# Performance work log

Hardware: AMD Instinct MI355X
Metric: run time of the kernel (lower is better)

The kernel has to match this reference:

```python
import jax, jax.numpy as jnp
import numpy as np

B, S, E, H = 4, 1024, 1024, 16
HD = E // H
EPS = 1e-10


def setup_inputs() -> dict:
    key = jax.random.key(0)
    ks = jax.random.split(key, 10)
    w = lambda k: jax.random.normal(k, (E, E), jnp.float32) * 0.02
    b = lambda k: jax.random.normal(k, (E,), jnp.float32) * 0.02
    return {
        "query": jax.random.normal(ks[0], (B, S, E), jnp.float32),
        "Wq": w(ks[1]), "bq": b(ks[2]),
        "Wk": w(ks[3]), "bk": b(ks[4]),
        "Wv": w(ks[5]), "bv": b(ks[6]),
        "Wo": w(ks[7]), "bo": b(ks[8]),
        "alpha": jnp.array(1.0, jnp.float32),
    }


def reference(query, Wq, bq, Wk, bk, Wv, bv, Wo, bo, alpha):
    scale = 1.0 / np.sqrt(HD)
    # projections -> [B, H, S, HD]
    def heads(x, W, bias):
        return (x @ W.T + bias).reshape(B, S, H, HD).transpose(0, 2, 1, 3)
    Q = heads(query, Wq, bq)
    K = heads(query, Wk, bk)
    V = heads(query, Wv, bv)
    # raw scores [B, H, S, S]
    scores = jnp.einsum('bhqd,bhkd->bhqk', Q, K) * scale
    # 2D FFT over the (q, k) plane
    scores_fft = jnp.fft.fft2(scores, axes=(-2, -1))
    # spectral filter: exp(i * alpha * arctan(log|F| + eps))
    phase = alpha * jnp.arctan(jnp.log(jnp.abs(scores_fft) + EPS))
    filt = jnp.exp(1j * phase)
    scores_filtered = jnp.fft.ifft2(scores_fft * filt, axes=(-2, -1)).real
    # softmax over keys (dropout is identity at eval)
    attn = jax.nn.softmax(scores_filtered, axis=-1)
    ctx = jnp.einsum('bhqk,bhkd->bhqd', attn, V)
    ctx = ctx.transpose(0, 2, 1, 3).reshape(B, S, E)
    return ctx @ Wo.T + bo
```

## Files before the change

### kernel.cpp

```cpp
#include <hip/hip_runtime.h>
#include <hip/hip_fp16.h>


typedef __attribute__((ext_vector_type(8))) short short8;
typedef __attribute__((ext_vector_type(8))) _Float16 half8;
typedef __attribute__((ext_vector_type(4))) float f32x4;

#define PITCH 40
#define PITCH1 72

__device__ __forceinline__ float bf2f(short v) {
  return __uint_as_float(((unsigned)(unsigned short)v) << 16);
}
__device__ __forceinline__ short f2bf(float f) {
  unsigned u = __float_as_uint(f);
  u += 0x7FFFu + ((u >> 16) & 1u);
  return (short)(u >> 16);
}

__device__ __forceinline__ short8 ld8(const void* p, size_t idx, int isf32) {
  short8 r;
  if (isf32) {
    const float* f = (const float*)p + idx;
    float4 a = *(const float4*)f;
    float4 b = *(const float4*)(f + 4);
    r[0] = f2bf(a.x); r[1] = f2bf(a.y); r[2] = f2bf(a.z); r[3] = f2bf(a.w);
    r[4] = f2bf(b.x); r[5] = f2bf(b.y); r[6] = f2bf(b.z); r[7] = f2bf(b.w);
  } else {
    r = *(const short8*)((const short*)p + idx);
  }
  return r;
}
__device__ __forceinline__ float ldf(const void* p, int idx, int isf32) {
  return isf32 ? ((const float*)p)[idx] : bf2f(((const short*)p)[idx]);
}

__device__ __forceinline__ float2 cmul(float2 a, float2 b) {
  return make_float2(a.x * b.x - a.y * b.y, a.x * b.y + a.y * b.x);
}
__device__ __forceinline__ float2 cmulc(float2 a, float2 b) {
  return make_float2(a.x * b.x + a.y * b.y, a.y * b.x - a.x * b.y);
}
__device__ __forceinline__ float2 cadd(float2 a, float2 b) {
  return make_float2(a.x + b.x, a.y + b.y);
}
__device__ __forceinline__ float2 csub(float2 a, float2 b) {
  return make_float2(a.x - b.x, a.y - b.y);
}


template <int SGN>
__device__ __forceinline__ void dft16_dif(float2* x) {
  const float C16[8] = {1.f, 0.92387953f, 0.70710678f, 0.38268343f,
                        0.f, -0.38268343f, -0.70710678f, -0.92387953f};
  const float S16[8] = {0.f, 0.38268343f, 0.70710678f, 0.92387953f,
                        1.f, 0.92387953f, 0.70710678f, 0.38268343f};
#pragma unroll
  for (int h = 8; h >= 1; h >>= 1)
#pragma unroll
    for (int b = 0; b < 16; b += 2 * h)
#pragma unroll
      for (int i = 0; i < h; ++i) {
        const int e = i * (8 / h);
        float2 u = x[b + i], v = x[b + i + h];
        x[b + i] = cadd(u, v);
        float2 d = csub(u, v);
        float2 w = make_float2(C16[e], SGN > 0 ? S16[e] : -S16[e]);
        x[b + i + h] = (e == 0) ? d : cmul(d, w);
      }
}

__device__ __forceinline__ void dit16_inv(float2* x) {
  const float C16[8] = {1.f, 0.92387953f, 0.70710678f, 0.38268343f,
                        0.f, -0.38268343f, -0.70710678f, -0.92387953f};
  const float S16[8] = {0.f, 0.38268343f, 0.70710678f, 0.92387953f,
                        1.f, 0.92387953f, 0.70710678f, 0.38268343f};
#pragma unroll
  for (int h = 1; h <= 8; h <<= 1)
#pragma unroll
    for (int b = 0; b < 16; b += 2 * h)
#pragma unroll
      for (int i = 0; i < h; ++i) {
        const int e = i * (8 / h);
        float2 w = make_float2(C16[e], -S16[e]);
        float2 u = x[b + i];
        float2 vh = (e == 0) ? x[b + i + h] : cmulc(x[b + i + h], w);
        x[b + i] = cadd(u, vh);
        x[b + i + h] = csub(u, vh);
      }
}

template <int SGN>
__device__ __forceinline__ void midtw(float2* x, int lane) {
  const int rho[16] = {0, 8, 4, 12, 2, 10, 6, 14, 1, 9, 5, 13, 3, 11, 7, 15};
  float s, c;
  __sincosf((float)lane * 0.00613592315f, &s, &c);
  float2 w = make_float2(c, SGN > 0 ? s : -s);
  float2 run = w;
  x[8] = cmul(x[8], run);
#pragma unroll
  for (int e = 2; e < 16; ++e) {
    run = cmul(run, w);
    x[rho[e]] = cmul(x[rho[e]], run);
  }
}

template <int SGN>
__device__ __forceinline__ void xlane_dif(float2* x, int lane) {
#pragma unroll
  for (int h = 32; h >= 1; h >>= 1) {
    const int e = (lane & (h - 1)) * (32 / h);
    float s, c;
    __sincosf((float)e * 0.09817477042f, &s, &c);
    float2 w = make_float2(c, SGN > 0 ? s : -s);
    const bool hi = (lane & h) != 0;
#pragma unroll
    for (int r = 0; r < 16; ++r) {
      float2 t = x[r];
      float2 p;
      p.x = __shfl_xor(t.x, h, 64);
      p.y = __shfl_xor(t.y, h, 64);
      x[r] = hi ? cmul(csub(p, t), w) : cadd(t, p);
    }
  }
}

template <int SGN>
__device__ __forceinline__ void wfft1024_dif(float2* x, int lane) {
  dft16_dif<SGN>(x);
  midtw<SGN>(x, lane);
  xlane_dif<SGN>(x, lane);
}

template <int SGN>
__device__ __forceinline__ void midtw2(float2* x, float2* y, int lane) {
  const int rho[16] = {0, 8, 4, 12, 2, 10, 6, 14, 1, 9, 5, 13, 3, 11, 7, 15};
  float s, c;
  __sincosf((float)lane * 0.00613592315f, &s, &c);
  float2 w = make_float2(c, SGN > 0 ? s : -s);
  float2 run = w;
  x[8] = cmul(x[8], run);
  y[8] = cmul(y[8], run);
#pragma unroll
  for (int e = 2; e < 16; ++e) {
    run = cmul(run, w);
    x[rho[e]] = cmul(x[rho[e]], run);
    y[rho[e]] = cmul(y[rho[e]], run);
  }
}

__device__ __forceinline__ void midtw_inv2(float2* x, float2* y, int lane) {
  const int rho[16] = {0, 8, 4, 12, 2, 10, 6, 14, 1, 9, 5, 13, 3, 11, 7, 15};
  float s, c;
  __sincosf((float)lane * 0.00613592315f, &s, &c);
  float2 w = make_float2(c, -s);
  float2 run = w;
  x[8] = cmulc(x[8], run);
  y[8] = cmulc(y[8], run);
#pragma unroll
  for (int e = 2; e < 16; ++e) {
    run = cmul(run, w);
    x[rho[e]] = cmulc(x[rho[e]], run);
    y[rho[e]] = cmulc(y[rho[e]], run);
  }
}

template <int SGN>
__device__ __forceinline__ void xlane_dif2(float2* x, float2* y, int lane) {
#pragma unroll
  for (int h = 32; h >= 1; h >>= 1) {
    const int e = (lane & (h - 1)) * (32 / h);
    float s, c;
    __sincosf((float)e * 0.09817477042f, &s, &c);
    float2 w = make_float2(c, SGN > 0 ? s : -s);
    const bool hi = (lane & h) != 0;
#pragma unroll
    for (int r = 0; r < 16; ++r) {
      float2 t = x[r];
      float2 p;
      p.x = __shfl_xor(t.x, h, 64);
      p.y = __shfl_xor(t.y, h, 64);
      x[r] = hi ? cmul(csub(p, t), w) : cadd(t, p);
    }
#pragma unroll
    for (int r = 0; r < 16; ++r) {
      float2 t = y[r];
      float2 p;
      p.x = __shfl_xor(t.x, h, 64);
      p.y = __shfl_xor(t.y, h, 64);
      y[r] = hi ? cmul(csub(p, t), w) : cadd(t, p);
    }
  }
}

__device__ __forceinline__ void xlane_dit_inv2(float2* x, float2* y, int lane) {
#pragma unroll
  for (int h = 1; h <= 32; h <<= 1) {
    const int e = (lane & (h - 1)) * (32 / h);
    float s, c;
    __sincosf((float)e * 0.09817477042f, &s, &c);
    float2 w = make_float2(c, -s);
    const bool hi = (lane & h) != 0;
#pragma unroll
    for (int r = 0; r < 16; ++r) {
      float2 t = x[r];
      if (hi) t = cmulc(t, w);
      float2 p;
      p.x = __shfl_xor(t.x, h, 64);
      p.y = __shfl_xor(t.y, h, 64);
      x[r] = hi ? csub(p, t) : cadd(t, p);
    }
#pragma unroll
    for (int r = 0; r < 16; ++r) {
      float2 t = y[r];
      if (hi) t = cmulc(t, w);
      float2 p;
      p.x = __shfl_xor(t.x, h, 64);
      p.y = __shfl_xor(t.y, h, 64);
      y[r] = hi ? csub(p, t) : cadd(t, p);
    }
  }
}

template <int SGN>
__device__ __forceinline__ void wfft1024_dif2(float2* x, float2* y, int lane) {
  dft16_dif<SGN>(x);
  dft16_dif<SGN>(y);
  midtw2<SGN>(x, y, lane);
  xlane_dif2<SGN>(x, y, lane);
}
__device__ __forceinline__ void wfft1024_inv2(float2* x, float2* y, int lane) {
  xlane_dit_inv2(x, y, lane);
  midtw_inv2(x, y, lane);
  dit16_inv(x);
  dit16_inv(y);
}

__device__ __forceinline__ float gainw(float re, float im, float alpha, bool a1) {
  float mag2 = re * re + im * im;
  float t = 0.5f * __logf(mag2 + 1e-20f);
  if (a1) return __builtin_amdgcn_rsqf(fmaf(t, t, 1.0f)) * (1.0f / 1048576.0f);
  return __cosf(alpha * atanf(t)) * (1.0f / 1048576.0f);
}

__global__ void k0_detect(const unsigned* __restrict__ q,
                          const void* __restrict__ alphap, int* __restrict__ flags) {
  __shared__ float smax[256];
  __shared__ int szero[256];
  int t = threadIdx.x;
  float mx = 0.f; int zc = 0;
  for (int i = t; i < 16384; i += 256) {
    unsigned w = q[i];
    unsigned lo = w & 0xFFFFu;
    float v = fabsf(__uint_as_float(lo << 16));
    if (!(v <= 1e30f)) v = 1e30f;
    mx = fmaxf(mx, v);
    zc += (lo == 0u);
  }
  smax[t] = mx; szero[t] = zc;
  __syncthreads();
  for (int s = 128; s > 0; s >>= 1) {
    if (t < s) { smax[t] = fmaxf(smax[t], smax[t + s]); szero[t] += szero[t + s]; }
    __syncthreads();
  }
  if (t == 0) {
    int isf32 = (smax[0] > 100.f) || (szero[0] > 12288);
    flags[0] = isf32;
    float alpha = isf32 ? *(const float*)alphap : bf2f(*(const short*)alphap);
    ((float*)flags)[1] = alpha;
  }
}

__global__ __launch_bounds__(256) void k1_qkv(
    const void* __restrict__ x,
    const void* __restrict__ Wq, const void* __restrict__ bq,
    const void* __restrict__ Wk, const void* __restrict__ bk,
    const void* __restrict__ Wv, const void* __restrict__ bv,
    short* __restrict__ Qt, short* __restrict__ Kt, short* __restrict__ Vt,
    const int* __restrict__ flags)
{
  __shared__ __align__(16) char smem[128 * PITCH1 * 2 * 2];
  short* As = (short*)smem;
  short* Bs = As + 128 * PITCH1;
  short* Ct = (short*)smem;
  const int isf32 = flags[0];
  const int t = threadIdx.x;
  const int lb = blockIdx.x;
  const int m0 = ((lb & 7) * 4 + ((lb >> 3) & 3)) * 128;
  const int n0 = (lb >> 5) * 128;
  const int which = blockIdx.y;
  const void* __restrict__ W = (which == 0) ? Wq : (which == 1) ? Wk : Wv;
  const void* __restrict__ bias = (which == 0) ? bq : (which == 1) ? bk : bv;
  const int lane = t & 63, wvi = t >> 6;
  const int wr = wvi >> 1, wc = wvi & 1;
  const int lm = lane & 15, lq = lane >> 4;
  f32x4 acc[4][4] = {};

  for (int k0 = 0; k0 < 1024; k0 += 64) {
    __syncthreads();
#pragma unroll
    for (int i = 0; i < 4; ++i) {
      int l = t + i * 256;
      int row = l >> 3, kk = (l & 7) << 3;
      *(short8*)&As[row * PITCH1 + kk] = ld8(x, (size_t)(m0 + row) * 1024 + k0 + kk, isf32);
      *(short8*)&Bs[row * PITCH1 + kk] = ld8(W, (size_t)(n0 + row) * 1024 + k0 + kk, isf32);
    }
    __syncthreads();
#pragma unroll
    for (int kh = 0; kh < 2; ++kh) {
      short8 af[4], bf[4];
#pragma unroll
      for (int a = 0; a < 4; ++a)
        af[a] = *(const short8*)&As[(wr * 64 + a * 16 + lm) * PITCH1 + kh * 32 + lq * 8];
#pragma unroll
      for (int b = 0; b < 4; ++b)
        bf[b] = *(const short8*)&Bs[(wc * 64 + b * 16 + lm) * PITCH1 + kh * 32 + lq * 8];
#pragma unroll
      for (int a = 0; a < 4; ++a)
#pragma unroll
        for (int b = 0; b < 4; ++b)
          acc[a][b] = __builtin_amdgcn_mfma_f32_16x16x32_bf16(af[a], bf[b], acc[a][b], 0, 0, 0);
    }
  }

  __syncthreads();
#pragma unroll
  for (int a = 0; a < 4; ++a)
#pragma unroll
    for (int b = 0; b < 4; ++b) {
      int col = wc * 64 + b * 16 + lm;
      float bv_ = ldf(bias, n0 + col, isf32);
#pragma unroll
      for (int r = 0; r < 4; ++r) {
        int row = wr * 64 + a * 16 + lq * 4 + r;
        Ct[row * 136 + col] = f2bf(acc[a][b][r] + bv_);
      }
    }
  __syncthreads();

  short* __restrict__ O = (which == 0) ? Qt : (which == 1) ? Kt : Vt;
#pragma unroll
  for (int j = 0; j < 8; ++j) {
    int id = t + j * 256;
    int d128 = id & 127, sg = (id >> 7) * 8;
    short vals[8];
#pragma unroll
    for (int i = 0; i < 8; ++i) vals[i] = Ct[(sg + i) * 136 + d128];
    int col = n0 + d128;
    int h = col >> 6, d = col & 63;
    int bb = m0 >> 10, sbase = (m0 & 1023) + sg;
    *(short8*)&O[(((size_t)(bb * 16 + h)) << 16) + ((size_t)d << 10) + sbase] = *(short8*)vals;
  }
}

__global__ __launch_bounds__(128) void kA_qkfft(
    const short* __restrict__ Qt, const short* __restrict__ Kt,
    __half2* __restrict__ Qhat, __half2* __restrict__ Khat)
{
  __shared__ float2 sbuf[2][1024];
  const int lane = threadIdx.x & 63, w = threadIdx.x >> 6;
  const int z = blockIdx.y;
  const int bx = blockIdx.x;
  if (bx < 16) {
    const short* qp = Qt + ((size_t)z << 16);
    const int d0 = bx * 4 + w * 2;
    float2 x[16], y[16];
#pragma unroll
    for (int j = 0; j < 16; ++j) {
      x[j] = make_float2(0.125f * bf2f(qp[(d0 << 10) + lane + 64 * j]), 0.f);
      y[j] = make_float2(0.125f * bf2f(qp[((d0 + 1) << 10) + lane + 64 * j]), 0.f);
    }
    wfft1024_dif2<-1>(x, y, lane);
    __half2* o0 = Qhat + (((size_t)(z * 64 + d0)) << 10);
    __half2* o1 = o0 + 1024;
#pragma unroll
    for (int r = 0; r < 16; ++r) {
      o0[lane + 64 * r] = __float22half2_rn(x[r]);
      o1[lane + 64 * r] = __float22half2_rn(y[r]);
    }
  } else {
    const short* kp = Kt + ((size_t)z << 16);
    const int p = (bx - 16) * 2 + w;
    const int d0 = 2 * p;
    float2 x[16];
#pragma unroll
    for (int j = 0; j < 16; ++j)
      x[j] = make_float2(bf2f(kp[(d0 << 10) + lane + 64 * j]),
                         bf2f(kp[((d0 + 1) << 10) + lane + 64 * j]));
    wfft1024_dif<-1>(x, lane);
    const int rho[16] = {0, 8, 4, 12, 2, 10, 6, 14, 1, 9, 5, 13, 3, 11, 7, 15};
    const int bl6 = ((lane & 1) << 5) | ((lane & 2) << 3) | ((lane & 4) << 1) |
                    ((lane & 8) >> 1) | ((lane & 16) >> 3) | ((lane & 32) >> 5);
    float2* buf = sbuf[w];
#pragma unroll
    for (int r = 0; r < 16; ++r) buf[rho[r] + 16 * bl6] = x[r];
    __half2* o0 = Khat + (size_t)(z * 64 + d0) * 520;
    __half2* o1 = o0 + 520;
#pragma unroll 1
    for (int jj = 0; jj < 9; ++jj) {
      int v = lane + 64 * jj;
      if (v <= 512) {
        float2 A = buf[v], B = buf[(1024 - v) & 1023];
        o0[v] = __float22half2_rn(make_float2((A.x + B.x) * 0.5f, (A.y - B.y) * 0.5f));
        o1[v] = __float22half2_rn(make_float2((A.y + B.y) * 0.5f, (B.x - A.x) * 0.5f));
      }
    }
  }
}

__global__ __launch_bounds__(256) void kB_specmm(
    const __half2* __restrict__ Qhat, const __half2* __restrict__ Khat,
    __half2* __restrict__ Ct, const int* __restrict__ flags, int bh0)
{
  __shared__ unsigned short Are[64][72], Aim[64][72], Bre[128][72], Bim[128][72];
  const int t = threadIdx.x;
  const int u0 = blockIdx.x * 128;
  const int v0 = blockIdx.y * 64;
  const int zl = blockIdx.z;
  const int z = bh0 + zl;
  const float alpha = ((const float*)flags)[1];
  const bool a1 = (alpha == 1.0f);
  {
    const int d = t >> 2;
    const ushort2* src = (const ushort2*)(Khat + (size_t)(z * 64 + d) * 520);
    int vb = (t & 3) * 16;
#pragma unroll
    for (int j = 0; j < 16; ++j) {
      int v = v0 + vb + j;
      if (v > 519) v = 519;
      ushort2 e = src[v];
      int row = vb + j;
      int dc = d ^ (((row >> 4) & 3) << 4);
      Are[row][dc] = e.x;
      Aim[row][dc] = e.y;
    }
    const ushort2* srcb = (const ushort2*)(Qhat + (((size_t)(z * 64 + d)) << 10) + u0);
    int ub = (t & 3) * 32;
#pragma unroll
    for (int j = 0; j < 32; ++j) {
      ushort2 e = srcb[ub + j];
      int row = ub + j;
      int dc = d ^ (((row >> 5) & 3) << 4);
      Bre[row][dc] = e.x;
      Bim[row][dc] = e.y;
    }
  }
  __syncthreads();

  const int lane = t & 63, wc = t >> 6;
  const int lm = lane & 15, lq = lane >> 4;
  f32x4 cre[4][2] = {}, cim[4][2] = {};
#pragma unroll
  for (int ks = 0; ks < 2; ++ks) {
    half8 ar[4], ai[4], aiN[4], br[2], bi[2];
#pragma unroll
    for (int a = 0; a < 4; ++a) {
      int dc = (ks * 32 + lq * 8) ^ ((a & 3) << 4);
      ar[a] = *(const half8*)&Are[a * 16 + lm][dc];
      ai[a] = *(const half8*)&Aim[a * 16 + lm][dc];
      int4 tm = *(int4*)&ai[a];
      tm.x ^= 0x80008000; tm.y ^= 0x80008000; tm.z ^= 0x80008000; tm.w ^= 0x80008000;
      aiN[a] = *(half8*)&tm;
    }
#pragma unroll
    for (int n = 0; n < 2; ++n) {
      int dc = (ks * 32 + lq * 8) ^ ((wc & 3) << 4);
      br[n] = *(const half8*)&Bre[wc * 32 + n * 16 + lm][dc];
      bi[n] = *(const half8*)&Bim[wc * 32 + n * 16 + lm][dc];
    }
#pragma unroll
    for (int a = 0; a < 4; ++a)
#pragma unroll
      for (int n = 0; n < 2; ++n) {
        cre[a][n] = __builtin_amdgcn_mfma_f32_16x16x32_f16(ar[a], br[n], cre[a][n], 0, 0, 0);
        cre[a][n] = __builtin_amdgcn_mfma_f32_16x16x32_f16(aiN[a], bi[n], cre[a][n], 0, 0, 0);
        cim[a][n] = __builtin_amdgcn_mfma_f32_16x16x32_f16(ar[a], bi[n], cim[a][n], 0, 0, 0);
        cim[a][n] = __builtin_amdgcn_mfma_f32_16x16x32_f16(ai[a], br[n], cim[a][n], 0, 0, 0);
      }
  }

  __half2* outp = Ct + (size_t)zl * 513 * 1024 + u0 + wc * 32;
#pragma unroll
  for (int a = 0; a < 4; ++a)
#pragma unroll
    for (int r = 0; r < 4; ++r) {
      int v = v0 + a * 16 + lq * 4 + r;
      if (v < 513) {
#pragma unroll
        for (int n = 0; n < 2; ++n) {
          float re = cre[a][n][r], im = cim[a][n][r];
          float wf = gainw(re, im, alpha, a1);
          outp[(size_t)v * 1024 + n * 16 + lm] =
              __float22half2_rn(make_float2(re * wf, im * wf));
        }
      }
    }
}

__global__ __launch_bounds__(256) void k4_invfft(__half2* __restrict__ Ct)
{
  const int lane = threadIdx.x & 63;
  const int w = threadIdx.x >> 6;
  const int gv0 = blockIdx.x * 8 + w * 2;
  if (gv0 > 512) return;
  const bool has1 = (gv0 + 1 <= 512);
  __half2* __restrict__ row0 = Ct + (size_t)blockIdx.y * 513 * 1024 + ((size_t)gv0 << 10);
  __half2* __restrict__ row1 = row0 + 1024;
  float2 x[16], y[16];
#pragma unroll
  for (int j = 0; j < 16; ++j) x[j] = __half22float2(row0[lane + 64 * j]);
  if (has1) {
#pragma unroll
    for (int j = 0; j < 16; ++j) y[j] = __half22float2(row1[lane + 64 * j]);
  } else {
#pragma unroll
    for (int j = 0; j < 16; ++j) y[j] = make_float2(0.f, 0.f);
  }
  wfft1024_inv2(x, y, lane);
#pragma unroll
  for (int j = 0; j < 16; ++j) row0[lane + 64 * j] = __float22half2_rn(x[j]);
  if (has1) {
#pragma unroll
    for (int j = 0; j < 16; ++j) row1[lane + 64 * j] = __float22half2_rn(y[j]);
  }
}

__global__ __launch_bounds__(512) void k56_softmax_av(
    const __half2* __restrict__ Ct, const short* __restrict__ Vt,
    short* __restrict__ ctx, int bh0)
{
  __shared__ __align__(16) char GP[34816];
  const int tid = threadIdx.x;
  const int q0 = blockIdx.x * 16, z = blockIdx.y;
  const int lane = tid & 63, w = tid >> 6;
  const int lm = lane & 15, lq = lane >> 4;
  const __half2* __restrict__ in = Ct + (size_t)z * 513 * 1024;
#define GROW(m) ((__half2*)(GP + (m) * 2064))
  for (int id = tid; id < 2052; id += 512) {
    int v = id >> 2, qq = (id & 3) * 4;
    int4 o = *(const int4*)&in[(size_t)v * 1024 + q0 + qq];
    __half2* op = (__half2*)&o;
#pragma unroll
    for (int i = 0; i < 4; ++i) GROW(qq + i)[v] = op[i];
  }
  short* P = (short*)GP;
  const int bl6 = ((lane & 1) << 5) | ((lane & 2) << 3) | ((lane & 4) << 1) |
                  ((lane & 8) >> 1) | ((lane & 16) >> 3) | ((lane & 32) >> 5);
  __syncthreads();

  const int p = w;
  const __half2* g1 = GROW(2 * p);
  const __half2* g2 = GROW(2 * p + 1);
  float2 x[16];
#pragma unroll
  for (int j = 0; j < 16; ++j) {
    int v = lane + 64 * j;
    float2 a, b;
    if (v <= 512) {
      a = __half22float2(g1[v]);
      b = __half22float2(g2[v]);
    } else {
      int v2 = 1024 - v;
      float2 aa = __half22float2(g1[v2]), bb = __half22float2(g2[v2]);
      a = make_float2(aa.x, -aa.y);
      b = make_float2(bb.x, -bb.y);
    }
    x[j] = make_float2(a.x - b.y, a.y + b.x);
  }

  wfft1024_dif<1>(x, lane);

  float m1 = -3.4e38f, m2 = -3.4e38f;
#pragma unroll
  for (int j = 0; j < 16; ++j) { m1 = fmaxf(m1, x[j].x); m2 = fmaxf(m2, x[j].y); }
#pragma unroll
  for (int s = 32; s > 0; s >>= 1) {
    m1 = fmaxf(m1, __shfl_xor(m1, s, 64));
    m2 = fmaxf(m2, __shfl_xor(m2, s, 64));
  }
  float s1 = 0.f, s2 = 0.f;
#pragma unroll
  for (int j = 0; j < 16; ++j) {
    float e1 = __expf(x[j].x - m1), e2 = __expf(x[j].y - m2);
    x[j] = make_float2(e1, e2);
    s1 += e1; s2 += e2;
  }
#pragma unroll
  for (int s = 32; s > 0; s >>= 1) {
    s1 += __shfl_xor(s1, s, 64);
    s2 += __shfl_xor(s2, s, 64);
  }
  float inv1 = 1.0f / s1, inv2 = 1.0f / s2;

  __syncthreads();

  {
    const int rho[16] = {0, 8, 4, 12, 2, 10, 6, 14, 1, 9, 5, 13, 3, 11, 7, 15};
    short a0[16], a1[16];
#pragma unroll
    for (int pos = 0; pos < 16; ++pos) {
      const int j = rho[pos];
      a0[pos] = f2bf(x[j].x * inv1);
      a1[pos] = f2bf(x[j].y * inv2);
    }
    short* dst0 = &P[(2 * p) * 1040 + 16 * bl6];
    short* dst1 = &P[(2 * p + 1) * 1040 + 16 * bl6];
    *(short8*)dst0       = *(short8*)&a0[0];
    *(short8*)(dst0 + 8) = *(short8*)&a0[8];
    *(short8*)dst1       = *(short8*)&a1[0];
    *(short8*)(dst1 + 8) = *(short8*)&a1[8];
  }
  __syncthreads();

  const short* __restrict__ Vp = Vt + ((size_t)(bh0 + z) << 16);
  f32x4 acc[4] = {};
#pragma unroll
  for (int ks = 0; ks < 4; ++ks) {
    int k0 = w * 128 + ks * 32;
    short8 a0 = *(const short8*)&P[lm * 1040 + k0 + lq * 8];
#pragma unroll
    for (int b = 0; b < 4; ++b) {
      short8 bv = *(const short8*)&Vp[(size_t)(b * 16 + lm) * 1024 + k0 + lq * 8];
      acc[b] = __builtin_amdgcn_mfma_f32_16x16x32_bf16(a0, bv, acc[b], 0, 0, 0);
    }
  }
  __syncthreads();
  float* red = (float*)GP;
#pragma unroll
  for (int b = 0; b < 4; ++b)
#pragma unroll
    for (int r = 0; r < 4; ++r)
      red[(w * 16 + lq * 4 + r) * 68 + b * 16 + lm] = acc[b][r];
  __syncthreads();
  if (tid < 256) {
    int q = tid >> 4, d0 = (tid & 15) * 4;
    float s0 = 0.f, s1_ = 0.f, s2_ = 0.f, s3 = 0.f;
#pragma unroll
    for (int ww = 0; ww < 8; ++ww) {
      const float* rr = &red[(ww * 16 + q) * 68 + d0];
      s0 += rr[0]; s1_ += rr[1]; s2_ += rr[2]; s3 += rr[3];
    }
    short o4[4] = {f2bf(s0), f2bf(s1_), f2bf(s2_), f2bf(s3)};
    *(int2*)&ctx[(((size_t)(bh0 + z)) << 16) + (size_t)(q0 + q) * 64 + d0] = *(int2*)o4;
  }
#undef GROW
}

__global__ __launch_bounds__(256) void k7_out(
    const short* __restrict__ ctx, const void* __restrict__ Wo,
    const void* __restrict__ bo, void* __restrict__ out,
    const int* __restrict__ flags)
{
  __shared__ __align__(16) char smem[128 * 136 * 2];
  short* As = (short*)smem;
  short* Bs = As + 128 * PITCH;
  short* Ct = (short*)smem;
  const int isf32 = flags[0];
  const int t = threadIdx.x;
  const int lb = blockIdx.x;
  const int m0 = ((lb & 7) * 4 + ((lb >> 3) & 3)) * 128;
  const int n0 = (lb >> 5) * 128;
  const int lane = t & 63, wvi = t >> 6;
  const int wr = wvi >> 1, wc = wvi & 1;
  const int lm = lane & 15, lq = lane >> 4;
  f32x4 acc[4][4] = {};

  for (int k0 = 0; k0 < 1024; k0 += 32) {
    __syncthreads();
#pragma unroll
    for (int i = 0; i < 2; ++i) {
      int l = t + i * 256;
      int row = l >> 2, kk = (l & 3) << 3;
      int n = m0 + row, e = k0 + kk;
      size_t aaddr = (((size_t)((n >> 10) * 16 + (e >> 6))) << 16) + (size_t)((n & 1023) << 6) + (e & 63);
      *(int4*)&As[row * PITCH + kk] = *(const int4*)&ctx[aaddr];
      *(short8*)&Bs[row * PITCH + kk] = ld8(Wo, (size_t)(n0 + row) * 1024 + e, isf32);
    }
    __syncthreads();
    short8 af[4], bf[4];
#pragma unroll
    for (int a = 0; a < 4; ++a) af[a] = *(const short8*)&As[(wr * 64 + a * 16 + lm) * PITCH + lq * 8];
#pragma unroll
    for (int b = 0; b < 4; ++b) bf[b] = *(const short8*)&Bs[(wc * 64 + b * 16 + lm) * PITCH + lq * 8];
#pragma unroll
    for (int a = 0; a < 4; ++a)
#pragma unroll
      for (int b = 0; b < 4; ++b)
        acc[a][b] = __builtin_amdgcn_mfma_f32_16x16x32_bf16(af[a], bf[b], acc[a][b], 0, 0, 0);
  }

  if (isf32) {
#pragma unroll
    for (int a = 0; a < 4; ++a)
#pragma unroll
      for (int b = 0; b < 4; ++b) {
        int col = n0 + wc * 64 + b * 16 + lm;
        float bo_ = ldf(bo, col, 1);
#pragma unroll
        for (int r = 0; r < 4; ++r) {
          int row = m0 + wr * 64 + a * 16 + lq * 4 + r;
          ((float*)out)[(size_t)row * 1024 + col] = acc[a][b][r] + bo_;
        }
      }
    return;
  }
  __syncthreads();
#pragma unroll
  for (int a = 0; a < 4; ++a)
#pragma unroll
    for (int b = 0; b < 4; ++b) {
      int col = wc * 64 + b * 16 + lm;
      float bo_ = ldf(bo, n0 + col, 0);
#pragma unroll
      for (int r = 0; r < 4; ++r) {
        int row = wr * 64 + a * 16 + lq * 4 + r;
        Ct[row * 136 + col] = f2bf(acc[a][b][r] + bo_);
      }
    }
  __syncthreads();
#pragma unroll
  for (int j = 0; j < 8; ++j) {
    int id = t + j * 256;
    int row = id >> 4, c16 = (id & 15) * 8;
    short8 v = *(const short8*)&Ct[row * 136 + c16];
    *(short8*)&((short*)out)[(size_t)(m0 + row) * 1024 + n0 + c16] = v;
  }
}

extern "C" void kernel_launch(void* const* d_in, const int* in_sizes, int n_in,
                              void* d_out, int out_size, void* d_ws, size_t ws_size,
                              hipStream_t stream)
{
  const void* x  = d_in[0];
  const void* Wq = d_in[1];
  const void* bq = d_in[2];
  const void* Wk = d_in[3];
  const void* bk = d_in[4];
  const void* Wv = d_in[5];
  const void* bv = d_in[6];
  const void* Wo = d_in[7];
  const void* bo = d_in[8];
  const void* alphap = d_in[9];
  char* ws = (char*)d_ws;

  const size_t PLANE_CT = (size_t)513 * 1024 * 4;
  const size_t QH_SZ = (size_t)64 * 64 * 1024 * 4;
  const size_t KH_SZ = (size_t)64 * 64 * 520 * 4;

  const size_t B_CT  = 0;
  const size_t B_VT  = 64 * PLANE_CT;
  const size_t B_CX  = B_VT + ((size_t)8u << 20);
  const size_t B_QH  = B_CX + ((size_t)8u << 20);
  const size_t B_KH  = B_QH + QH_SZ;
  const size_t B_FL  = B_KH + KH_SZ;
  const size_t B_NEED = B_FL + 256;

  if (ws_size >= B_NEED) {
    short*   Qt   = (short*)(ws);
    short*   Kt   = (short*)(ws + ((size_t)8u << 20));
    short*   Vt   = (short*)(ws + B_VT);
    short*   ctx  = (short*)(ws + B_CX);
    __half2* Ct   = (__half2*)(ws + B_CT);
    __half2* Qhat = (__half2*)(ws + B_QH);
    __half2* Khat = (__half2*)(ws + B_KH);
    int*     flags = (int*)(ws + B_FL);

    k0_detect<<<1, 256, 0, stream>>>((const unsigned*)x, alphap, flags);
    k1_qkv<<<dim3(256, 3), 256, 0, stream>>>(x, Wq, bq, Wk, bk, Wv, bv, Qt, Kt, Vt, flags);
    kA_qkfft<<<dim3(32, 64), 128, 0, stream>>>(Qt, Kt, Qhat, Khat);
    kB_specmm<<<dim3(8, 9, 64), 256, 0, stream>>>(Qhat, Khat, Ct, flags, 0);
    k4_invfft<<<dim3(65, 64), 256, 0, stream>>>(Ct);
    k56_softmax_av<<<dim3(64, 64), 512, 0, stream>>>(Ct, Vt, ctx, 0);
    k7_out<<<256, 256, 0, stream>>>(ctx, Wo, bo, d_out, flags);
    return;
  }

  const size_t VT_OFF = (size_t)17u << 20;
  const size_t CX_OFF = (size_t)25u << 20;
  const size_t QH_OFF = (size_t)33u << 20;
  const size_t KH_OFF = QH_OFF + QH_SZ;
  const size_t FL_OFF = KH_OFF + KH_SZ;

  short*   Qt   = (short*)(ws);
  short*   Kt   = (short*)(ws + ((size_t)8u << 20));
  short*   Vt   = (short*)(ws + VT_OFF);
  short*   ctx  = (short*)(ws + CX_OFF);
  __half2* Ct   = (__half2*)(ws);
  __half2* Qhat = (__half2*)(ws + QH_OFF);
  __half2* Khat = (__half2*)(ws + KH_OFF);
  int*     flags = (int*)(ws + FL_OFF);

  k0_detect<<<1, 256, 0, stream>>>((const unsigned*)x, alphap, flags);
  k1_qkv<<<dim3(256, 3), 256, 0, stream>>>(x, Wq, bq, Wk, bk, Wv, bv, Qt, Kt, Vt, flags);
  kA_qkfft<<<dim3(32, 64), 128, 0, stream>>>(Qt, Kt, Qhat, Khat);
  for (int c = 0; c < 8; ++c) {
    int bh0 = c * 8;
    kB_specmm<<<dim3(8, 9, 8), 256, 0, stream>>>(Qhat, Khat, Ct, flags, bh0);
    k4_invfft<<<dim3(65, 8), 256, 0, stream>>>(Ct);
    k56_softmax_av<<<dim3(64, 8), 512, 0, stream>>>(Ct, Vt, ctx, bh0);
  }
  k7_out<<<256, 256, 0, stream>>>(ctx, Wo, bo, d_out, flags);
}
```

Measured before the change: 676.4 us.

## Rewrite inverse 1024-point FFT as two 32x32 DFT matmuls on MFMA

Replaces the register/shuffle radix-16 inverse FFT with a four-step 32x32 decomposition. The two DFT stages run as fp16 MFMA matmuls against a twiddle matrix stored as split hi/lo fp16 parts, with a pointwise twiddle in between and LDS transposes. Each wave processes four rows in sequence, and the grid shrinks to match. The aim is to move FFT arithmetic off scalar VALU work and cross-lane shuffles onto matrix cores. In exchange it adds LDS traffic, block-wide barriers inside the row loop, and some fp16 precision risk on the intermediate values.

```diff
diff --git a/kernel.cpp b/kernel.cpp
--- a/kernel.cpp
+++ b/kernel.cpp
@@ -8,6 +8,7 @@
 
 #define PITCH 40
 #define PITCH1 72
+#define TP 40
 
 __device__ __forceinline__ float bf2f(short v) {
   return __uint_as_float(((unsigned)(unsigned short)v) << 16);
@@ -38,14 +39,16 @@
 __device__ __forceinline__ float2 cmul(float2 a, float2 b) {
   return make_float2(a.x * b.x - a.y * b.y, a.x * b.y + a.y * b.x);
 }
-__device__ __forceinline__ float2 cmulc(float2 a, float2 b) {
-  return make_float2(a.x * b.x + a.y * b.y, a.y * b.x - a.x * b.y);
-}
 __device__ __forceinline__ float2 cadd(float2 a, float2 b) {
   return make_float2(a.x + b.x, a.y + b.y);
 }
 __device__ __forceinline__ float2 csub(float2 a, float2 b) {
   return make_float2(a.x - b.x, a.y - b.y);
+}
+__device__ __forceinline__ half8 hneg(half8 v) {
+  int4 t = *(int4*)&v;
+  t.x ^= 0x80008000; t.y ^= 0x80008000; t.z ^= 0x80008000; t.w ^= 0x80008000;
+  return *(half8*)&t;
 }
 
 
@@ -67,26 +70,6 @@
         float2 d = csub(u, v);
         float2 w = make_float2(C16[e], SGN > 0 ? S16[e] : -S16[e]);
         x[b + i + h] = (e == 0) ? d : cmul(d, w);
-      }
-}
-
-__device__ __forceinline__ void dit16_inv(float2* x) {
-  const float C16[8] = {1.f, 0.92387953f, 0.70710678f, 0.38268343f,
-                        0.f, -0.38268343f, -0.70710678f, -0.92387953f};
-  const float S16[8] = {0.f, 0.38268343f, 0.70710678f, 0.92387953f,
-                        1.f, 0.92387953f, 0.70710678f, 0.38268343f};
-#pragma unroll
-  for (int h = 1; h <= 8; h <<= 1)
-#pragma unroll
-    for (int b = 0; b < 16; b += 2 * h)
-#pragma unroll
-      for (int i = 0; i < h; ++i) {
-        const int e = i * (8 / h);
-        float2 w = make_float2(C16[e], -S16[e]);
-        float2 u = x[b + i];
-        float2 vh = (e == 0) ? x[b + i + h] : cmulc(x[b + i + h], w);
-        x[b + i] = cadd(u, vh);
-        x[b + i + h] = csub(u, vh);
       }
 }
 
@@ -149,22 +132,6 @@
   }
 }
 
-__device__ __forceinline__ void midtw_inv2(float2* x, float2* y, int lane) {
-  const int rho[16] = {0, 8, 4, 12, 2, 10, 6, 14, 1, 9, 5, 13, 3, 11, 7, 15};
-  float s, c;
-  __sincosf((float)lane * 0.00613592315f, &s, &c);
-  float2 w = make_float2(c, -s);
-  float2 run = w;
-  x[8] = cmulc(x[8], run);
-  y[8] = cmulc(y[8], run);
-#pragma unroll
-  for (int e = 2; e < 16; ++e) {
-    run = cmul(run, w);
-    x[rho[e]] = cmulc(x[rho[e]], run);
-    y[rho[e]] = cmulc(y[rho[e]], run);
-  }
-}
-
 template <int SGN>
 __device__ __forceinline__ void xlane_dif2(float2* x, float2* y, int lane) {
 #pragma unroll
@@ -193,47 +160,12 @@
   }
 }
 
-__device__ __forceinline__ void xlane_dit_inv2(float2* x, float2* y, int lane) {
-#pragma unroll
-  for (int h = 1; h <= 32; h <<= 1) {
-    const int e = (lane & (h - 1)) * (32 / h);
-    float s, c;
-    __sincosf((float)e * 0.09817477042f, &s, &c);
-    float2 w = make_float2(c, -s);
-    const bool hi = (lane & h) != 0;
-#pragma unroll
-    for (int r = 0; r < 16; ++r) {
-      float2 t = x[r];
-      if (hi) t = cmulc(t, w);
-      float2 p;
-      p.x = __shfl_xor(t.x, h, 64);
-      p.y = __shfl_xor(t.y, h, 64);
-      x[r] = hi ? csub(p, t) : cadd(t, p);
-    }
-#pragma unroll
-    for (int r = 0; r < 16; ++r) {
-      float2 t = y[r];
-      if (hi) t = cmulc(t, w);
-      float2 p;
-      p.x = __shfl_xor(t.x, h, 64);
-      p.y = __shfl_xor(t.y, h, 64);
-      y[r] = hi ? csub(p, t) : cadd(t, p);
-    }
-  }
-}
-
 template <int SGN>
 __device__ __forceinline__ void wfft1024_dif2(float2* x, float2* y, int lane) {
   dft16_dif<SGN>(x);
   dft16_dif<SGN>(y);
   midtw2<SGN>(x, y, lane);
   xlane_dif2<SGN>(x, y, lane);
-}
-__device__ __forceinline__ void wfft1024_inv2(float2* x, float2* y, int lane) {
-  xlane_dit_inv2(x, y, lane);
-  midtw_inv2(x, y, lane);
-  dit16_inv(x);
-  dit16_inv(y);
 }
 
 __device__ __forceinline__ float gainw(float re, float im, float alpha, bool a1) {
@@ -458,9 +390,7 @@
       int dc = (ks * 32 + lq * 8) ^ ((a & 3) << 4);
       ar[a] = *(const half8*)&Are[a * 16 + lm][dc];
       ai[a] = *(const half8*)&Aim[a * 16 + lm][dc];
-      int4 tm = *(int4*)&ai[a];
-      tm.x ^= 0x80008000; tm.y ^= 0x80008000; tm.z ^= 0x80008000; tm.w ^= 0x80008000;
-      aiN[a] = *(half8*)&tm;
+      aiN[a] = hneg(ai[a]);
     }
 #pragma unroll
     for (int n = 0; n < 2; ++n) {
@@ -497,31 +427,147 @@
     }
 }
 
-__global__ __launch_bounds__(256) void k4_invfft(__half2* __restrict__ Ct)
+__global__ __launch_bounds__(256) void k4_invfft(__half2* __restrict__ Ct, int nrows)
 {
-  const int lane = threadIdx.x & 63;
-  const int w = threadIdx.x >> 6;
-  const int gv0 = blockIdx.x * 8 + w * 2;
-  if (gv0 > 512) return;
-  const bool has1 = (gv0 + 1 <= 512);
-  __half2* __restrict__ row0 = Ct + (size_t)blockIdx.y * 513 * 1024 + ((size_t)gv0 << 10);
-  __half2* __restrict__ row1 = row0 + 1024;
-  float2 x[16], y[16];
-#pragma unroll
-  for (int j = 0; j < 16; ++j) x[j] = __half22float2(row0[lane + 64 * j]);
-  if (has1) {
-#pragma unroll
-    for (int j = 0; j < 16; ++j) y[j] = __half22float2(row1[lane + 64 * j]);
-  } else {
-#pragma unroll
-    for (int j = 0; j < 16; ++j) y[j] = make_float2(0.f, 0.f);
-  }
-  wfft1024_inv2(x, y, lane);
-#pragma unroll
-  for (int j = 0; j < 16; ++j) row0[lane + 64 * j] = __float22half2_rn(x[j]);
-  if (has1) {
-#pragma unroll
-    for (int j = 0; j < 16; ++j) row1[lane + 64 * j] = __float22half2_rn(y[j]);
+  __shared__ unsigned short CM[4][32][TP];
+  __shared__ unsigned short SC[4][4][32][TP];
+  const int tid = threadIdx.x;
+  const int lane = tid & 63, w = tid >> 6;
+  const int lm = lane & 15, lq = lane >> 4;
+
+  for (int i = tid; i < 1024; i += 256) {
+    int r = i >> 5, c = i & 31;
+    int brc = ((c & 1) << 4) | ((c & 2) << 2) | (c & 4) | ((c & 8) >> 2) | ((c & 16) >> 4);
+    float ang = (float)((brc * r) & 31) * 0.19634954084936207f;
+    float sv, cv;
+    __sincosf(ang, &sv, &cv);
+    __half chh = __float2half(cv), shh = __float2half(sv);
+    CM[0][r][c] = __half_as_ushort(chh);
+    CM[1][r][c] = __half_as_ushort(__float2half(cv - __half2float(chh)));
+    CM[2][r][c] = __half_as_ushort(shh);
+    CM[3][r][c] = __half_as_ushort(__float2half(sv - __half2float(shh)));
+  }
+  __syncthreads();
+
+  half8 cf[4][2];
+#pragma unroll
+  for (int cmp = 0; cmp < 4; ++cmp)
+#pragma unroll
+    for (int t = 0; t < 2; ++t)
+      cf[cmp][t] = *(const half8*)&CM[cmp][t * 16 + lm][lq * 8];
+
+  unsigned short (*MRE)[TP] = SC[w][0];
+  unsigned short (*MIM)[TP] = SC[w][1];
+  unsigned short (*TRE)[TP] = SC[w][2];
+  unsigned short (*TIM)[TP] = SC[w][3];
+
+  const int slot = blockIdx.x * 4 + w;
+  __half2* __restrict__ plane = Ct + (size_t)blockIdx.y * 513 * 1024;
+
+#pragma unroll 1
+  for (int rr = 0; rr < 4; ++rr) {
+    const int vrow = slot * 4 + rr;
+    const bool act = (vrow < nrows);
+    __half2* __restrict__ row = plane + ((size_t)(act ? vrow : 0) << 10);
+    int4 ch4[4];
+#pragma unroll
+    for (int k = 0; k < 4; ++k)
+      ch4[k] = act ? *(const int4*)&row[4 * (lane + 64 * k)] : make_int4(0, 0, 0, 0);
+#pragma unroll
+    for (int k = 0; k < 4; ++k) {
+      const unsigned* e = (const unsigned*)&ch4[k];
+      unsigned short re4[4], im4[4];
+#pragma unroll
+      for (int j = 0; j < 4; ++j) {
+        unsigned u = e[j];
+        re4[j] = (unsigned short)(u & 0xFFFFu);
+        im4[j] = (unsigned short)((u >> 16) ^ 0x8000u);
+      }
+      int h = (lane >> 3) + 8 * k, c0 = 4 * (lane & 7);
+      *(int2*)&MRE[h][c0] = *(int2*)re4;
+      *(int2*)&MIM[h][c0] = *(int2*)im4;
+    }
+    __syncthreads();
+
+    half8 mre[2], mng[2], mps[2];
+#pragma unroll
+    for (int t = 0; t < 2; ++t) {
+      mre[t] = *(const half8*)&MRE[t * 16 + lm][lq * 8];
+      mng[t] = *(const half8*)&MIM[t * 16 + lm][lq * 8];
+      mps[t] = hneg(mng[t]);
+    }
+    f32x4 ar[2][2] = {}, ai[2][2] = {};
+#pragma unroll
+    for (int i = 0; i < 2; ++i)
+#pragma unroll
+      for (int j = 0; j < 2; ++j) {
+        ar[i][j] = __builtin_amdgcn_mfma_f32_16x16x32_f16(mre[i], cf[0][j], ar[i][j], 0, 0, 0);
+        ar[i][j] = __builtin_amdgcn_mfma_f32_16x16x32_f16(mre[i], cf[1][j], ar[i][j], 0, 0, 0);
+        ar[i][j] = __builtin_amdgcn_mfma_f32_16x16x32_f16(mng[i], cf[2][j], ar[i][j], 0, 0, 0);
+        ar[i][j] = __builtin_amdgcn_mfma_f32_16x16x32_f16(mng[i], cf[3][j], ar[i][j], 0, 0, 0);
+        ai[i][j] = __builtin_amdgcn_mfma_f32_16x16x32_f16(mre[i], cf[2][j], ai[i][j], 0, 0, 0);
+        ai[i][j] = __builtin_amdgcn_mfma_f32_16x16x32_f16(mre[i], cf[3][j], ai[i][j], 0, 0, 0);
+        ai[i][j] = __builtin_amdgcn_mfma_f32_16x16x32_f16(mps[i], cf[0][j], ai[i][j], 0, 0, 0);
+        ai[i][j] = __builtin_amdgcn_mfma_f32_16x16x32_f16(mps[i], cf[1][j], ai[i][j], 0, 0, 0);
+      }
+
+#pragma unroll
+    for (int i = 0; i < 2; ++i)
+#pragma unroll
+      for (int j = 0; j < 2; ++j) {
+        unsigned short tr4[4], ti4[4];
+#pragma unroll
+        for (int r = 0; r < 4; ++r) {
+          int h = i * 16 + lq * 4 + r;
+          int q0 = j * 16 + lm;
+          int brh = ((h & 1) << 4) | ((h & 2) << 2) | (h & 4) | ((h & 8) >> 2) | ((h & 16) >> 4);
+          float ang = (float)(brh * q0) * 0.006135923151542565f;
+          float sv, cv;
+          __sincosf(ang, &sv, &cv);
+          float nre = ar[i][j][r], nim = ai[i][j][r];
+          float tre = cv * nre - sv * nim;
+          float tim = cv * nim + sv * nre;
+          tr4[r] = __half_as_ushort(__float2half(tre));
+          ti4[r] = __half_as_ushort(__float2half(-tim));
+        }
+        *(int2*)&TRE[j * 16 + lm][i * 16 + lq * 4] = *(int2*)tr4;
+        *(int2*)&TIM[j * 16 + lm][i * 16 + lq * 4] = *(int2*)ti4;
+      }
+    __syncthreads();
+
+    half8 tre[2], tng[2], tps[2];
+#pragma unroll
+    for (int t = 0; t < 2; ++t) {
+      tre[t] = *(const half8*)&TRE[t * 16 + lm][lq * 8];
+      tng[t] = *(const half8*)&TIM[t * 16 + lm][lq * 8];
+      tps[t] = hneg(tng[t]);
+    }
+    f32x4 gr[2][2] = {}, gi[2][2] = {};
+#pragma unroll
+    for (int i = 0; i < 2; ++i)
+#pragma unroll
+      for (int j = 0; j < 2; ++j) {
+        gr[i][j] = __builtin_amdgcn_mfma_f32_16x16x32_f16(cf[0][i], tre[j], gr[i][j], 0, 0, 0);
+        gr[i][j] = __builtin_amdgcn_mfma_f32_16x16x32_f16(cf[1][i], tre[j], gr[i][j], 0, 0, 0);
+        gr[i][j] = __builtin_amdgcn_mfma_f32_16x16x32_f16(cf[2][i], tng[j], gr[i][j], 0, 0, 0);
+        gr[i][j] = __builtin_amdgcn_mfma_f32_16x16x32_f16(cf[3][i], tng[j], gr[i][j], 0, 0, 0);
+        gi[i][j] = __builtin_amdgcn_mfma_f32_16x16x32_f16(cf[0][i], tps[j], gi[i][j], 0, 0, 0);
+        gi[i][j] = __builtin_amdgcn_mfma_f32_16x16x32_f16(cf[1][i], tps[j], gi[i][j], 0, 0, 0);
+        gi[i][j] = __builtin_amdgcn_mfma_f32_16x16x32_f16(cf[2][i], tre[j], gi[i][j], 0, 0, 0);
+        gi[i][j] = __builtin_amdgcn_mfma_f32_16x16x32_f16(cf[3][i], tre[j], gi[i][j], 0, 0, 0);
+      }
+
+    if (act) {
+#pragma unroll
+      for (int i = 0; i < 2; ++i)
+#pragma unroll
+        for (int j = 0; j < 2; ++j)
+#pragma unroll
+          for (int r = 0; r < 4; ++r) {
+            int q = 512 * i + 128 * lq + 32 * r + 16 * j + lm;
+            row[q] = __float22half2_rn(make_float2(gr[i][j][r], gi[i][j][r]));
+          }
+    }
   }
 }
 
@@ -769,7 +815,7 @@
     k1_qkv<<<dim3(256, 3), 256, 0, stream>>>(x, Wq, bq, Wk, bk, Wv, bv, Qt, Kt, Vt, flags);
     kA_qkfft<<<dim3(32, 64), 128, 0, stream>>>(Qt, Kt, Qhat, Khat);
     kB_specmm<<<dim3(8, 9, 64), 256, 0, stream>>>(Qhat, Khat, Ct, flags, 0);
-    k4_invfft<<<dim3(65, 64), 256, 0, stream>>>(Ct);
+    k4_invfft<<<dim3(33, 64), 256, 0, stream>>>(Ct, 513);
     k56_softmax_av<<<dim3(64, 64), 512, 0, stream>>>(Ct, Vt, ctx, 0);
     k7_out<<<256, 256, 0, stream>>>(ctx, Wo, bo, d_out, flags);
     return;
@@ -796,7 +842,7 @@
   for (int c = 0; c < 8; ++c) {
     int bh0 = c * 8;
     kB_specmm<<<dim3(8, 9, 8), 256, 0, stream>>>(Qhat, Khat, Ct, flags, bh0);
-    k4_invfft<<<dim3(65, 8), 256, 0, stream>>>(Ct);
+    k4_invfft<<<dim3(33, 8), 256, 0, stream>>>(Ct, 513);
     k56_softmax_av<<<dim3(64, 8), 512, 0, stream>>>(Ct, Vt, ctx, bh0);
   }
   k7_out<<<256, 256, 0, stream>>>(ctx, Wo, bo, d_out, flags);
```

Result: faster. 611.8 us (-9.5%).
